# Kernel tuning notes

Hardware: AMD Instinct MI355X
Metric: run time of the kernel (lower is better)

Reference implementation:

```python
import jax, jax.numpy as jnp
import numpy as np

N_NODES = 50000


def gcn_conv(x, src, dst, W, b, n):
    # PyG GCNConv: h = x @ W; out[i] = sum_j norm_ij * h[j] + b, with added self-loops
    h = x @ W  # [N, out]
    deg = jax.ops.segment_sum(jnp.ones_like(dst, dtype=h.dtype), dst, num_segments=n)
    inv_sqrt_deg = jnp.where(deg > 0, jax.lax.rsqrt(deg), 0.0)  # [N]
    coeff = inv_sqrt_deg[src] * inv_sqrt_deg[dst]  # [E]
    msg = h[src] * coeff[:, None]  # [E, out] gather (memory-bound)
    out = jax.ops.segment_sum(msg, dst, num_segments=n)  # scatter-add
    return out + b


def setup_inputs() -> dict:
    key = jax.random.key(0)
    ks = jax.random.split(key, 8)
    n, e, c_in, c_hid, c_out = N_NODES, 800000, 128, 128, 64
    x = jax.random.normal(ks[0], (n, c_in), dtype=jnp.float32)
    edge_index = jax.random.randint(ks[1], (2, e), 0, n, dtype=jnp.int64)
    # Glorot-ish scaled weights
    W1 = jax.random.normal(ks[2], (c_in, c_hid), dtype=jnp.float32) / np.sqrt(c_in)
    b1 = jnp.zeros((c_hid,), dtype=jnp.float32)
    W2 = jax.random.normal(ks[3], (c_hid, c_out), dtype=jnp.float32) / np.sqrt(c_hid)
    b2 = jnp.zeros((c_out,), dtype=jnp.float32)
    lin_W = jax.random.normal(ks[4], (2 * c_out, c_out), dtype=jnp.float32) / np.sqrt(2 * c_out)
    lin_b = jnp.zeros((c_out,), dtype=jnp.float32)
    return {"x": x, "edge_index": edge_index, "W1": W1, "b1": b1,
            "W2": W2, "b2": b2, "lin_W": lin_W, "lin_b": lin_b}


def reference(x, edge_index, W1, b1, W2, b2, lin_W, lin_b):
    n = x.shape[0]
    # add self-loops (as GCNConv does by default)
    loops = jnp.arange(n, dtype=edge_index.dtype)
    src = jnp.concatenate([edge_index[0], loops])
    dst = jnp.concatenate([edge_index[1], loops])

    def branch(x):
        h = jax.nn.relu(gcn_conv(x, src, dst, W1, b1, n))
        # dropout: identity in eval mode (training=False)
        return gcn_conv(h, src, dst, W2, b2, n)

    x1 = branch(x)
    x2 = branch(x)
    # FusionMethod == 'Concat'
    fused = jnp.concatenate([x1, x2], axis=1) @ lin_W + lin_b
    return jax.nn.log_softmax(fused, axis=1)
```

## Files before the change

kernel.cpp:

```cpp
#include <hip/hip_runtime.h>


#define CIN  128
#define CHID 128
#define COUT 64
#define BCAP_SH 13
#define BINCHUNK 2048
#define CELLCAP 32
#define ENTCAP  5120

typedef short v8s __attribute__((ext_vector_type(8)));
typedef float v4f __attribute__((ext_vector_type(4)));

static __device__ __forceinline__ unsigned short f2bf(float f) {
    unsigned int u = __float_as_uint(f);
    unsigned int r = (u + 0x7fffu + ((u >> 16) & 1u)) >> 16;
    return (unsigned short)r;
}
static __device__ __forceinline__ float bflo(unsigned int u) {
    return __uint_as_float(u << 16);
}
static __device__ __forceinline__ float bfhi(unsigned int u) {
    return __uint_as_float(u & 0xffff0000u);
}
static __device__ __forceinline__ unsigned int pk2(float a, float b) {
    return (unsigned int)f2bf(a) | ((unsigned int)f2bf(b) << 16);
}

__global__ __launch_bounds__(256) void bin_wprep_kernel(
        const int* __restrict__ src, const int* __restrict__ dst,
        int* __restrict__ cnt, unsigned int* __restrict__ binned, int E, int nchunk,
        const float* __restrict__ W1, const float* __restrict__ W2,
        const float* __restrict__ b2, const float* __restrict__ linW,
        const float* __restrict__ linb, unsigned short* __restrict__ Wt1,
        unsigned short* __restrict__ Wt2, float* __restrict__ bp) {
    int bb = blockIdx.x;
    int t = threadIdx.x;
    if (bb < nchunk) {
        __shared__ int h[256];
        __shared__ int cur[256];
        h[t] = 0;
        __syncthreads();
        int e0 = bb * BINCHUNK;
        int e1 = e0 + BINCHUNK; if (e1 > E) e1 = E;
        for (int e = e0 + t; e < e1; e += 256)
            atomicAdd(&h[dst[e] >> 8], 1);
        __syncthreads();
        int c = h[t];
        cnt[bb * 256 + t] = c < CELLCAP ? c : CELLCAP;
        cur[t] = 0;
        __syncthreads();
        for (int e = e0 + t; e < e1; e += 256) {
            int d = dst[e];
            int b = d >> 8;
            int pos = atomicAdd(&cur[b], 1);
            if (pos < CELLCAP)
                binned[((size_t)(bb * 256 + b)) * CELLCAP + pos] =
                    (unsigned int)src[e] | (((unsigned int)d & 255u) << 16);
        }
    } else {
        int wb = bb - nchunk;
        if (wb < CHID) {
            if (t < 128) {
                Wt1[wb * CIN + t] = f2bf(W1[t * CHID + wb]);
                if (t < COUT) {
                    float acc = 0.f;
#pragma unroll 8
                    for (int k = 0; k < COUT; ++k) {
                        float wsv = linW[k * COUT + t] + linW[(k + COUT) * COUT + t];
                        acc = fmaf(W2[wb * COUT + k], wsv, acc);
                    }
                    Wt2[t * CHID + wb] = f2bf(acc);
                }
            }
        } else {
            if (t < COUT) {
                float acc = 0.f;
#pragma unroll 8
                for (int k = 0; k < COUT; ++k) {
                    float wsv = linW[k * COUT + t] + linW[(k + COUT) * COUT + t];
                    acc = fmaf(b2[k], wsv, acc);
                }
                bp[t] = acc + linb[t];
            }
        }
    }
}

__global__ __launch_bounds__(512) void csr_gemm1_kernel(
        const unsigned int* __restrict__ binned, const int* __restrict__ cnt,
        int nchunk, int nbkt,
        int2* __restrict__ rowpair, float* __restrict__ inv,
        unsigned short* __restrict__ ebuf16,
        const float* __restrict__ x, const unsigned short* __restrict__ Wt1,
        unsigned short* __restrict__ h1t, int n) {
    int t = threadIdx.x;
    if ((int)blockIdx.x < nbkt) {
        int b = blockIdx.x;
        __shared__ int cc[512];
        __shared__ int ps[512];
        __shared__ unsigned int ent[ENTCAP];
        __shared__ int h[256];
        __shared__ int s2[256];
        int v = (t < nchunk) ? cnt[t * 256 + b] : 0;
        cc[t] = v;
        ps[t] = v;
        __syncthreads();
        for (int off = 1; off < 512; off <<= 1) {
            int u = (t >= off) ? ps[t - off] : 0;
            __syncthreads();
            ps[t] += u;
            __syncthreads();
        }
        int total = ps[511];
        if (total > ENTCAP) total = ENTCAP;
        if (t < nchunk && v > 0) {
            int basei = ps[t] - v;
            const unsigned int* cell = binned + ((size_t)(t * 256 + b)) * CELLCAP;
            for (int i = 0; i < v; ++i)
                if (basei + i < ENTCAP) ent[basei + i] = cell[i];
        }
        if (t < 256) h[t] = 0;
        __syncthreads();
        for (int i = t; i < total; i += 512)
            atomicAdd(&h[ent[i] >> 16], 1);
        __syncthreads();
        int myc = (t < 256) ? h[t] : 0;
        if (t < 256) s2[t] = myc;
        __syncthreads();
        for (int off = 1; off < 256; off <<= 1) {
            int u = (t >= off && t < 256) ? s2[t - off] : 0;
            __syncthreads();
            if (t < 256) s2[t] += u;
            __syncthreads();
        }
        int base = b << BCAP_SH;
        if (t < 256) {
            int excl = s2[t] - myc;
            int node = (b << 8) + t;
            if (node < n) {
                rowpair[node] = make_int2(base + excl, base + excl + myc);
                inv[node] = rsqrtf((float)(myc + 1));
            }
            h[t] = base + excl;
        }
        __syncthreads();
        for (int i = t; i < total; i += 512) {
            unsigned int e = ent[i];
            int pos = atomicAdd(&h[e >> 16], 1);
            ebuf16[pos] = (unsigned short)(e & 0xffffu);
        }
    } else {
        int bid = blockIdx.x - nbkt;
        int lane = t & 63, wave = t >> 6;
        int quad = lane >> 4, r16 = lane & 15;
        int row0 = (bid * 8 + wave) * 16;
        if (row0 >= n) return;
        int arow = row0 + r16;
        if (arow >= n) arow = n - 1;
        size_t n32 = (size_t)n * 32;

        v4f acc[8];
#pragma unroll
        for (int c = 0; c < 8; ++c) acc[c] = (v4f){0.f, 0.f, 0.f, 0.f};
#pragma unroll
        for (int kc = 0; kc < 4; ++kc) {
            const float4* ap = (const float4*)(x + (size_t)arow * 128 + kc * 32 + quad * 8);
            float4 a0 = ap[0], a1 = ap[1];
            v8s af;
            af[0] = (short)f2bf(a0.x); af[1] = (short)f2bf(a0.y);
            af[2] = (short)f2bf(a0.z); af[3] = (short)f2bf(a0.w);
            af[4] = (short)f2bf(a1.x); af[5] = (short)f2bf(a1.y);
            af[6] = (short)f2bf(a1.z); af[7] = (short)f2bf(a1.w);
#pragma unroll
            for (int ct = 0; ct < 8; ++ct) {
                v8s bf = *(const v8s*)(Wt1 + (size_t)(ct * 16 + r16) * 128 + kc * 32 + quad * 8);
                acc[ct] = __builtin_amdgcn_mfma_f32_16x16x32_bf16(af, bf, acc[ct], 0, 0, 0);
            }
        }
#pragma unroll
        for (int ct = 0; ct < 8; ++ct) {
            int col = ct * 16 + r16;
            int pl = col >> 5, d = col & 31;
#pragma unroll
            for (int i = 0; i < 4; ++i) {
                int orow = row0 + quad * 4 + i;
                if (orow < n)
                    h1t[(size_t)pl * n32 + (size_t)orow * 32 + d] = f2bf(acc[ct][i]);
            }
        }
    }
}

__global__ __launch_bounds__(256) void agg1_slice_kernel(
        const unsigned short* __restrict__ h1t,
        const unsigned short* __restrict__ ebuf16,
        const int2* __restrict__ rowpair,
        const float* __restrict__ inv,
        const float* __restrict__ b1,
        unsigned int* __restrict__ agg1b,
        int n) {
    int b = blockIdx.x;
    int xcd = b & 7;
    int slice = xcd >> 1;
    int sub = xcd & 1;
    int grp = b >> 3;
    int wid = threadIdx.x >> 6;
    int lane = threadIdx.x & 63;
    int g = lane >> 3, s = lane & 7;
    const uint2* __restrict__ plane = (const uint2*)(h1t + (size_t)slice * n * 32);

    int node = (grp * 2 + sub) * 32 + wid * 8 + g;
    int cnode = node < n ? node : n - 1;
    int2 rp = rowpair[cnode];
    int beg = rp.x, len = rp.y - rp.x;
    int m = len < 64 ? len : 64;
    uint2 usl = plane[(size_t)cnode * 8 + s];
    float wd = inv[cnode];
    float4 bv = ((const float4*)b1)[slice * 8 + s];

    int kmax = (m + 1) & ~1;
    float a0 = 0.f, a1 = 0.f, a2 = 0.f, a3 = 0.f;
    int g8 = g << 3;
    int eid = 0;
    for (int k = 0; k < kmax; k += 2) {
        if ((k & 7) == 0) eid = (int)ebuf16[beg + k + s];
        int sa = __shfl(eid, g8 + (k & 7), 64);
        int sb = __shfl(eid, g8 + (k & 7) + 1, 64);
        sb = (k + 1 < m) ? sb : cnode;
        float iva = inv[sa], ivb = inv[sb];
        uint2 ua = plane[(size_t)sa * 8 + s];
        uint2 ub = plane[(size_t)sb * 8 + s];
        a0 = fmaf(iva, bflo(ua.x), a0); a1 = fmaf(iva, bfhi(ua.x), a1);
        a2 = fmaf(iva, bflo(ua.y), a2); a3 = fmaf(iva, bfhi(ua.y), a3);
        a0 = fmaf(ivb, bflo(ub.x), a0); a1 = fmaf(ivb, bfhi(ub.x), a1);
        a2 = fmaf(ivb, bflo(ub.y), a2); a3 = fmaf(ivb, bfhi(ub.y), a3);
    }
    if (len > 64) {
        for (int k = 64; k < len; ++k) {
            int sid = (int)ebuf16[beg + k];
            float iv2 = inv[sid];
            uint2 u = plane[(size_t)sid * 8 + s];
            a0 = fmaf(iv2, bflo(u.x), a0); a1 = fmaf(iv2, bfhi(u.x), a1);
            a2 = fmaf(iv2, bflo(u.y), a2); a3 = fmaf(iv2, bfhi(u.y), a3);
        }
    }
    float c2 = (1.0f - (float)(kmax - m)) * wd;
    a0 = fmaf(c2, bflo(usl.x), a0); a1 = fmaf(c2, bfhi(usl.x), a1);
    a2 = fmaf(c2, bflo(usl.y), a2); a3 = fmaf(c2, bfhi(usl.y), a3);
    float o0 = fmaxf(fmaf(wd, a0, bv.x), 0.f);
    float o1 = fmaxf(fmaf(wd, a1, bv.y), 0.f);
    float o2 = fmaxf(fmaf(wd, a2, bv.z), 0.f);
    float o3 = fmaxf(fmaf(wd, a3, bv.w), 0.f);
    if (node < n) {
        uint2 w; w.x = pk2(o0, o1); w.y = pk2(o2, o3);
        ((uint2*)agg1b)[(size_t)node * 32 + slice * 8 + s] = w;
    }
}

__global__ __launch_bounds__(256) void gemm2_kernel(const unsigned short* __restrict__ A,
                                                    const unsigned short* __restrict__ Wt,
                                                    const float* __restrict__ inv,
                                                    unsigned short* __restrict__ h2t, int n) {
    int lane = threadIdx.x & 63;
    int wave = threadIdx.x >> 6;
    int quad = lane >> 4, r16 = lane & 15;
    int row0 = (blockIdx.x * 4 + wave) * 16;
    if (row0 >= n) return;
    int arow = row0 + r16;
    if (arow >= n) arow = n - 1;

    v4f acc[4];
#pragma unroll
    for (int c = 0; c < 4; ++c) acc[c] = (v4f){0.f, 0.f, 0.f, 0.f};
#pragma unroll
    for (int kc = 0; kc < 4; ++kc) {
        v8s af = *(const v8s*)(A + (size_t)arow * 128 + kc * 32 + quad * 8);
#pragma unroll
        for (int ct = 0; ct < 4; ++ct) {
            v8s bf = *(const v8s*)(Wt + (size_t)(ct * 16 + r16) * 128 + kc * 32 + quad * 8);
            acc[ct] = __builtin_amdgcn_mfma_f32_16x16x32_bf16(af, bf, acc[ct], 0, 0, 0);
        }
    }
    float4 iv = ((const float4*)(inv + row0))[quad];
#pragma unroll
    for (int ct = 0; ct < 4; ++ct) {
#pragma unroll
        for (int i = 0; i < 4; ++i) {
            int orow = row0 + quad * 4 + i;
            if (orow < n) {
                float sc = (i == 0) ? iv.x : (i == 1) ? iv.y : (i == 2) ? iv.z : iv.w;
                h2t[(size_t)orow * 64 + ct * 16 + r16] = f2bf(acc[ct][i] * sc);
            }
        }
    }
}

__global__ __launch_bounds__(256) void agg2_softmax_kernel(
        const unsigned short* __restrict__ h2t,
        const unsigned short* __restrict__ ebuf16,
        const int2* __restrict__ rowpair,
        const float* __restrict__ inv,
        const float* __restrict__ bp,
        float* __restrict__ outp, int n) {
    int wid = threadIdx.x >> 6;
    int lane = threadIdx.x & 63;
    int g = lane >> 3, s = lane & 7;
    int node = blockIdx.x * 32 + wid * 8 + g;
    int cnode = node < n ? node : n - 1;
    int2 rp = rowpair[cnode];
    int beg = rp.x, len = rp.y - rp.x;
    int m = len < 64 ? len : 64;
    const uint4* __restrict__ rows = (const uint4*)h2t;
    uint4 usl = rows[(size_t)cnode * 8 + s];
    float wd = inv[cnode];

    int kmax = (m + 1) & ~1;
    float a0 = 0.f, a1 = 0.f, a2 = 0.f, a3 = 0.f;
    float a4 = 0.f, a5 = 0.f, a6 = 0.f, a7 = 0.f;
    int g8 = g << 3;
    int eid = 0;
    for (int k = 0; k < kmax; k += 2) {
        if ((k & 7) == 0) eid = (int)ebuf16[beg + k + s];
        int sa = __shfl(eid, g8 + (k & 7), 64);
        int sb = __shfl(eid, g8 + (k & 7) + 1, 64);
        sb = (k + 1 < m) ? sb : cnode;
        uint4 ua = rows[(size_t)sa * 8 + s];
        uint4 ub = rows[(size_t)sb * 8 + s];
        a0 += bflo(ua.x); a1 += bfhi(ua.x); a2 += bflo(ua.y); a3 += bfhi(ua.y);
        a4 += bflo(ua.z); a5 += bfhi(ua.z); a6 += bflo(ua.w); a7 += bfhi(ua.w);
        a0 += bflo(ub.x); a1 += bfhi(ub.x); a2 += bflo(ub.y); a3 += bfhi(ub.y);
        a4 += bflo(ub.z); a5 += bfhi(ub.z); a6 += bflo(ub.w); a7 += bfhi(ub.w);
    }
    if (len > 64) {
        for (int k = 64; k < len; ++k) {
            int sid = (int)ebuf16[beg + k];
            uint4 u = rows[(size_t)sid * 8 + s];
            a0 += bflo(u.x); a1 += bfhi(u.x); a2 += bflo(u.y); a3 += bfhi(u.y);
            a4 += bflo(u.z); a5 += bfhi(u.z); a6 += bflo(u.w); a7 += bfhi(u.w);
        }
    }
    float c2 = 1.0f - (float)(kmax - m);
    a0 = fmaf(c2, bflo(usl.x), a0); a1 = fmaf(c2, bfhi(usl.x), a1);
    a2 = fmaf(c2, bflo(usl.y), a2); a3 = fmaf(c2, bfhi(usl.y), a3);
    a4 = fmaf(c2, bflo(usl.z), a4); a5 = fmaf(c2, bfhi(usl.z), a5);
    a6 = fmaf(c2, bflo(usl.w), a6); a7 = fmaf(c2, bfhi(usl.w), a7);
    float4 bpa = ((const float4*)bp)[s * 2];
    float4 bpb = ((const float4*)bp)[s * 2 + 1];
    float f0 = fmaf(wd, a0, bpa.x), f1 = fmaf(wd, a1, bpa.y);
    float f2 = fmaf(wd, a2, bpa.z), f3 = fmaf(wd, a3, bpa.w);
    float f4 = fmaf(wd, a4, bpb.x), f5 = fmaf(wd, a5, bpb.y);
    float f6 = fmaf(wd, a6, bpb.z), f7 = fmaf(wd, a7, bpb.w);
    float mx = fmaxf(fmaxf(fmaxf(f0, f1), fmaxf(f2, f3)),
                     fmaxf(fmaxf(f4, f5), fmaxf(f6, f7)));
    mx = fmaxf(mx, __shfl_xor(mx, 1, 64));
    mx = fmaxf(mx, __shfl_xor(mx, 2, 64));
    mx = fmaxf(mx, __shfl_xor(mx, 4, 64));
    float sum = expf(f0 - mx) + expf(f1 - mx) + expf(f2 - mx) + expf(f3 - mx)
              + expf(f4 - mx) + expf(f5 - mx) + expf(f6 - mx) + expf(f7 - mx);
    sum += __shfl_xor(sum, 1, 64);
    sum += __shfl_xor(sum, 2, 64);
    sum += __shfl_xor(sum, 4, 64);
    float ls = mx + logf(sum);
    if (node < n) {
        float4 w0 = make_float4(f0 - ls, f1 - ls, f2 - ls, f3 - ls);
        float4 w1 = make_float4(f4 - ls, f5 - ls, f6 - ls, f7 - ls);
        ((float4*)outp)[(size_t)node * 16 + s * 2]     = w0;
        ((float4*)outp)[(size_t)node * 16 + s * 2 + 1] = w1;
    }
}

static inline size_t align16(size_t x) { return (x + 15) & ~(size_t)15; }

extern "C" void kernel_launch(void* const* d_in, const int* in_sizes, int n_in,
                              void* d_out, int out_size, void* d_ws, size_t ws_size,
                              hipStream_t stream) {
    const float* x    = (const float*)d_in[0];
    const int*   eidx = (const int*)d_in[1];
    const float* W1   = (const float*)d_in[2];
    const float* b1   = (const float*)d_in[3];
    const float* W2   = (const float*)d_in[4];
    const float* b2   = (const float*)d_in[5];
    const float* linW = (const float*)d_in[6];
    const float* linb = (const float*)d_in[7];
    float* out = (float*)d_out;

    const int n = in_sizes[0] / CIN;
    const int E = in_sizes[1] / 2;
    const int* src = eidx;
    const int* dst = eidx + E;
    const int NBKT = (n + 255) >> 8;
    const int NCHUNK = (E + BINCHUNK - 1) / BINCHUNK;

    char* ws = (char*)d_ws;
    size_t off = 0;
    int2*  rowpair = (int2*)(ws + off);  off = align16(off + (size_t)n * 8);
    float* inv     = (float*)(ws + off); off = align16(off + (size_t)n * 4);
    int*   cnt     = (int*)(ws + off);   off = align16(off + (size_t)NCHUNK * 256 * 4);
    unsigned short* Wt1 = (unsigned short*)(ws + off); off = align16(off + (size_t)CHID * CIN * 2);
    unsigned short* Wt2 = (unsigned short*)(ws + off); off = align16(off + (size_t)COUT * CHID * 2);
    float* bp      = (float*)(ws + off); off = align16(off + (size_t)COUT * 4);
    unsigned int* binned = (unsigned int*)(ws + off);
    off = align16(off + (size_t)NCHUNK * 256 * CELLCAP * 4);
    unsigned short* ebuf16 = (unsigned short*)(ws + off);
    off = align16(off + (size_t)256 * (1 << BCAP_SH) * 2);
    unsigned short* h1t   = (unsigned short*)(ws + off); off = align16(off + (size_t)n * CHID * 2);
    unsigned int*   agg1b = (unsigned int*)(ws + off);   off = align16(off + (size_t)n * CHID * 2);
    unsigned short* h2t   = (unsigned short*)(ws + off); off = align16(off + (size_t)n * COUT * 2);

    bin_wprep_kernel<<<NCHUNK + CHID + 1, 256, 0, stream>>>(
        src, dst, cnt, binned, E, NCHUNK, W1, W2, b2, linW, linb, Wt1, Wt2, bp);

    const int G1B = (n + 127) / 128;
    csr_gemm1_kernel<<<NBKT + G1B, 512, 0, stream>>>(
        binned, cnt, NCHUNK, NBKT, rowpair, inv, ebuf16, x, Wt1, h1t, n);

    const int NG1 = (n + 63) / 64;
    agg1_slice_kernel<<<NG1 * 8, 256, 0, stream>>>(h1t, ebuf16, rowpair, inv, b1, agg1b, n);

    gemm2_kernel<<<(n + 63) / 64, 256, 0, stream>>>((const unsigned short*)agg1b, Wt2, inv, h2t, n);

    agg2_softmax_kernel<<<(n + 31) / 32, 256, 0, stream>>>(h2t, ebuf16, rowpair, inv, bp, out, n);
}
```

Measured before the change: 191.6 us.

## Split CSR and GEMM1 kernels, prescale h1 rows by inverse sqrt degree

Separates the fused CSR-build and first GEMM into two launches so GEMM1 can run after the inverse-sqrt-degree array is ready. GEMM1 then multiplies each output row by its source normalisation, which lets the first aggregation drop the per-neighbour inv[] gather and just sum rows. The aggregation loop is widened to four neighbours per iteration to expose more memory parallelism. The cost is an extra kernel launch and serialisation that removes the overlap the fused kernel had between CSR construction and GEMM1.

```diff
diff --git a/kernel.cpp b/kernel.cpp
--- a/kernel.cpp
+++ b/kernel.cpp
@@ -73,120 +73,120 @@
                     Wt2[t * CHID + wb] = f2bf(acc);
                 }
             }
-        } else {
-            if (t < COUT) {
-                float acc = 0.f;
+        } else if (t < COUT) {
+            float acc = 0.f;
 #pragma unroll 8
-                for (int k = 0; k < COUT; ++k) {
-                    float wsv = linW[k * COUT + t] + linW[(k + COUT) * COUT + t];
-                    acc = fmaf(b2[k], wsv, acc);
-                }
-                bp[t] = acc + linb[t];
+            for (int k = 0; k < COUT; ++k) {
+                float wsv = linW[k * COUT + t] + linW[(k + COUT) * COUT + t];
+                acc = fmaf(b2[k], wsv, acc);
             }
-        }
-    }
-}
-
-__global__ __launch_bounds__(512) void csr_gemm1_kernel(
+            bp[t] = acc + linb[t];
+        }
+    }
+}
+
+__global__ __launch_bounds__(512) void csr_kernel(
         const unsigned int* __restrict__ binned, const int* __restrict__ cnt,
-        int nchunk, int nbkt,
+        int nchunk,
         int2* __restrict__ rowpair, float* __restrict__ inv,
-        unsigned short* __restrict__ ebuf16,
-        const float* __restrict__ x, const unsigned short* __restrict__ Wt1,
-        unsigned short* __restrict__ h1t, int n) {
+        unsigned short* __restrict__ ebuf16, int n) {
+    int b = blockIdx.x;
     int t = threadIdx.x;
-    if ((int)blockIdx.x < nbkt) {
-        int b = blockIdx.x;
-        __shared__ int cc[512];
-        __shared__ int ps[512];
-        __shared__ unsigned int ent[ENTCAP];
-        __shared__ int h[256];
-        __shared__ int s2[256];
-        int v = (t < nchunk) ? cnt[t * 256 + b] : 0;
-        cc[t] = v;
-        ps[t] = v;
-        __syncthreads();
-        for (int off = 1; off < 512; off <<= 1) {
-            int u = (t >= off) ? ps[t - off] : 0;
-            __syncthreads();
-            ps[t] += u;
-            __syncthreads();
-        }
-        int total = ps[511];
-        if (total > ENTCAP) total = ENTCAP;
-        if (t < nchunk && v > 0) {
-            int basei = ps[t] - v;
-            const unsigned int* cell = binned + ((size_t)(t * 256 + b)) * CELLCAP;
-            for (int i = 0; i < v; ++i)
-                if (basei + i < ENTCAP) ent[basei + i] = cell[i];
-        }
-        if (t < 256) h[t] = 0;
-        __syncthreads();
-        for (int i = t; i < total; i += 512)
-            atomicAdd(&h[ent[i] >> 16], 1);
-        __syncthreads();
-        int myc = (t < 256) ? h[t] : 0;
-        if (t < 256) s2[t] = myc;
-        __syncthreads();
-        for (int off = 1; off < 256; off <<= 1) {
-            int u = (t >= off && t < 256) ? s2[t - off] : 0;
-            __syncthreads();
-            if (t < 256) s2[t] += u;
-            __syncthreads();
-        }
-        int base = b << BCAP_SH;
-        if (t < 256) {
-            int excl = s2[t] - myc;
-            int node = (b << 8) + t;
-            if (node < n) {
-                rowpair[node] = make_int2(base + excl, base + excl + myc);
-                inv[node] = rsqrtf((float)(myc + 1));
-            }
-            h[t] = base + excl;
-        }
-        __syncthreads();
-        for (int i = t; i < total; i += 512) {
-            unsigned int e = ent[i];
-            int pos = atomicAdd(&h[e >> 16], 1);
-            ebuf16[pos] = (unsigned short)(e & 0xffffu);
-        }
-    } else {
-        int bid = blockIdx.x - nbkt;
-        int lane = t & 63, wave = t >> 6;
-        int quad = lane >> 4, r16 = lane & 15;
-        int row0 = (bid * 8 + wave) * 16;
-        if (row0 >= n) return;
-        int arow = row0 + r16;
-        if (arow >= n) arow = n - 1;
-        size_t n32 = (size_t)n * 32;
-
-        v4f acc[8];
-#pragma unroll
-        for (int c = 0; c < 8; ++c) acc[c] = (v4f){0.f, 0.f, 0.f, 0.f};
-#pragma unroll
-        for (int kc = 0; kc < 4; ++kc) {
-            const float4* ap = (const float4*)(x + (size_t)arow * 128 + kc * 32 + quad * 8);
-            float4 a0 = ap[0], a1 = ap[1];
-            v8s af;
-            af[0] = (short)f2bf(a0.x); af[1] = (short)f2bf(a0.y);
-            af[2] = (short)f2bf(a0.z); af[3] = (short)f2bf(a0.w);
-            af[4] = (short)f2bf(a1.x); af[5] = (short)f2bf(a1.y);
-            af[6] = (short)f2bf(a1.z); af[7] = (short)f2bf(a1.w);
-#pragma unroll
-            for (int ct = 0; ct < 8; ++ct) {
-                v8s bf = *(const v8s*)(Wt1 + (size_t)(ct * 16 + r16) * 128 + kc * 32 + quad * 8);
-                acc[ct] = __builtin_amdgcn_mfma_f32_16x16x32_bf16(af, bf, acc[ct], 0, 0, 0);
-            }
-        }
+    __shared__ int ps[512];
+    __shared__ unsigned int ent[ENTCAP];
+    __shared__ int h[256];
+    __shared__ int s2[256];
+    int v = (t < nchunk) ? cnt[t * 256 + b] : 0;
+    ps[t] = v;
+    __syncthreads();
+    for (int off = 1; off < 512; off <<= 1) {
+        int u = (t >= off) ? ps[t - off] : 0;
+        __syncthreads();
+        ps[t] += u;
+        __syncthreads();
+    }
+    int total = ps[511];
+    if (total > ENTCAP) total = ENTCAP;
+    if (t < nchunk && v > 0) {
+        int basei = ps[t] - v;
+        const unsigned int* cell = binned + ((size_t)(t * 256 + b)) * CELLCAP;
+        for (int i = 0; i < v; ++i)
+            if (basei + i < ENTCAP) ent[basei + i] = cell[i];
+    }
+    if (t < 256) h[t] = 0;
+    __syncthreads();
+    for (int i = t; i < total; i += 512)
+        atomicAdd(&h[ent[i] >> 16], 1);
+    __syncthreads();
+    int myc = (t < 256) ? h[t] : 0;
+    if (t < 256) s2[t] = myc;
+    __syncthreads();
+    for (int off = 1; off < 256; off <<= 1) {
+        int u = (t >= off && t < 256) ? s2[t - off] : 0;
+        __syncthreads();
+        if (t < 256) s2[t] += u;
+        __syncthreads();
+    }
+    int base = b << BCAP_SH;
+    if (t < 256) {
+        int excl = s2[t] - myc;
+        int node = (b << 8) + t;
+        if (node < n) {
+            rowpair[node] = make_int2(base + excl, base + excl + myc);
+            inv[node] = rsqrtf((float)(myc + 1));
+        }
+        h[t] = base + excl;
+    }
+    __syncthreads();
+    for (int i = t; i < total; i += 512) {
+        unsigned int e = ent[i];
+        int pos = atomicAdd(&h[e >> 16], 1);
+        ebuf16[pos] = (unsigned short)(e & 0xffffu);
+    }
+}
+
+__global__ __launch_bounds__(256) void gemm1_kernel(const float* __restrict__ A,
+                                                    const unsigned short* __restrict__ Wt,
+                                                    const float* __restrict__ inv,
+                                                    unsigned short* __restrict__ h1t, int n) {
+    int lane = threadIdx.x & 63;
+    int wave = threadIdx.x >> 6;
+    int quad = lane >> 4, r16 = lane & 15;
+    int row0 = (blockIdx.x * 4 + wave) * 16;
+    if (row0 >= n) return;
+    int arow = row0 + r16;
+    if (arow >= n) arow = n - 1;
+    size_t n32 = (size_t)n * 32;
+
+    v4f acc[8];
+#pragma unroll
+    for (int c = 0; c < 8; ++c) acc[c] = (v4f){0.f, 0.f, 0.f, 0.f};
+#pragma unroll
+    for (int kc = 0; kc < 4; ++kc) {
+        const float4* ap = (const float4*)(A + (size_t)arow * 128 + kc * 32 + quad * 8);
+        float4 a0 = ap[0], a1 = ap[1];
+        v8s af;
+        af[0] = (short)f2bf(a0.x); af[1] = (short)f2bf(a0.y);
+        af[2] = (short)f2bf(a0.z); af[3] = (short)f2bf(a0.w);
+        af[4] = (short)f2bf(a1.x); af[5] = (short)f2bf(a1.y);
+        af[6] = (short)f2bf(a1.z); af[7] = (short)f2bf(a1.w);
 #pragma unroll
         for (int ct = 0; ct < 8; ++ct) {
-            int col = ct * 16 + r16;
-            int pl = col >> 5, d = col & 31;
-#pragma unroll
-            for (int i = 0; i < 4; ++i) {
-                int orow = row0 + quad * 4 + i;
-                if (orow < n)
-                    h1t[(size_t)pl * n32 + (size_t)orow * 32 + d] = f2bf(acc[ct][i]);
+            v8s bf = *(const v8s*)(Wt + (size_t)(ct * 16 + r16) * 128 + kc * 32 + quad * 8);
+            acc[ct] = __builtin_amdgcn_mfma_f32_16x16x32_bf16(af, bf, acc[ct], 0, 0, 0);
+        }
+    }
+    float4 iv = ((const float4*)(inv + row0))[quad];
+#pragma unroll
+    for (int ct = 0; ct < 8; ++ct) {
+        int col = ct * 16 + r16;
+        int pl = col >> 5, d = col & 31;
+#pragma unroll
+        for (int i = 0; i < 4; ++i) {
+            int orow = row0 + quad * 4 + i;
+            if (orow < n) {
+                float sc = (i == 0) ? iv.x : (i == 1) ? iv.y : (i == 2) ? iv.z : iv.w;
+                h1t[(size_t)pl * n32 + (size_t)orow * 32 + d] = f2bf(acc[ct][i] * sc);
             }
         }
     }
@@ -208,6 +208,7 @@
     int wid = threadIdx.x >> 6;
     int lane = threadIdx.x & 63;
     int g = lane >> 3, s = lane & 7;
+    int g8 = g << 3;
     const uint2* __restrict__ plane = (const uint2*)(h1t + (size_t)slice * n * 32);
 
     int node = (grp * 2 + sub) * 32 + wid * 8 + g;
@@ -219,35 +220,38 @@
     float wd = inv[cnode];
     float4 bv = ((const float4*)b1)[slice * 8 + s];
 
-    int kmax = (m + 1) & ~1;
+    int kmax = (m + 3) & ~3;
     float a0 = 0.f, a1 = 0.f, a2 = 0.f, a3 = 0.f;
-    int g8 = g << 3;
     int eid = 0;
-    for (int k = 0; k < kmax; k += 2) {
+    for (int k = 0; k < kmax; k += 4) {
         if ((k & 7) == 0) eid = (int)ebuf16[beg + k + s];
-        int sa = __shfl(eid, g8 + (k & 7), 64);
-        int sb = __shfl(eid, g8 + (k & 7) + 1, 64);
-        sb = (k + 1 < m) ? sb : cnode;
-        float iva = inv[sa], ivb = inv[sb];
-        uint2 ua = plane[(size_t)sa * 8 + s];
-        uint2 ub = plane[(size_t)sb * 8 + s];
-        a0 = fmaf(iva, bflo(ua.x), a0); a1 = fmaf(iva, bfhi(ua.x), a1);
-        a2 = fmaf(iva, bflo(ua.y), a2); a3 = fmaf(iva, bfhi(ua.y), a3);
-        a0 = fmaf(ivb, bflo(ub.x), a0); a1 = fmaf(ivb, bfhi(ub.x), a1);
-        a2 = fmaf(ivb, bflo(ub.y), a2); a3 = fmaf(ivb, bfhi(ub.y), a3);
+        int i0 = __shfl(eid, g8 + (k & 7) + 0, 64);
+        int i1 = __shfl(eid, g8 + (k & 7) + 1, 64);
+        int i2 = __shfl(eid, g8 + (k & 7) + 2, 64);
+        int i3 = __shfl(eid, g8 + (k & 7) + 3, 64);
+        i0 = (k     < m) ? i0 : cnode;
+        i1 = (k + 1 < m) ? i1 : cnode;
+        i2 = (k + 2 < m) ? i2 : cnode;
+        i3 = (k + 3 < m) ? i3 : cnode;
+        uint2 u0 = plane[(size_t)i0 * 8 + s];
+        uint2 u1 = plane[(size_t)i1 * 8 + s];
+        uint2 u2 = plane[(size_t)i2 * 8 + s];
+        uint2 u3 = plane[(size_t)i3 * 8 + s];
+        a0 += bflo(u0.x); a1 += bfhi(u0.x); a2 += bflo(u0.y); a3 += bfhi(u0.y);
+        a0 += bflo(u1.x); a1 += bfhi(u1.x); a2 += bflo(u1.y); a3 += bfhi(u1.y);
+        a0 += bflo(u2.x); a1 += bfhi(u2.x); a2 += bflo(u2.y); a3 += bfhi(u2.y);
+        a0 += bflo(u3.x); a1 += bfhi(u3.x); a2 += bflo(u3.y); a3 += bfhi(u3.y);
     }
     if (len > 64) {
         for (int k = 64; k < len; ++k) {
             int sid = (int)ebuf16[beg + k];
-            float iv2 = inv[sid];
-            uint2 u = plane[(size_t)sid * 8 + s];
-            a0 = fmaf(iv2, bflo(u.x), a0); a1 = fmaf(iv2, bfhi(u.x), a1);
-            a2 = fmaf(iv2, bflo(u.y), a2); a3 = fmaf(iv2, bfhi(u.y), a3);
-        }
-    }
-    float c2 = (1.0f - (float)(kmax - m)) * wd;
-    a0 = fmaf(c2, bflo(usl.x), a0); a1 = fmaf(c2, bfhi(usl.x), a1);
-    a2 = fmaf(c2, bflo(usl.y), a2); a3 = fmaf(c2, bfhi(usl.y), a3);
+            uint2 uu = plane[(size_t)sid * 8 + s];
+            a0 += bflo(uu.x); a1 += bfhi(uu.x); a2 += bflo(uu.y); a3 += bfhi(uu.y);
+        }
+    }
+    float cc = 1.0f - (float)(kmax - m);
+    a0 = fmaf(cc, bflo(usl.x), a0); a1 = fmaf(cc, bfhi(usl.x), a1);
+    a2 = fmaf(cc, bflo(usl.y), a2); a3 = fmaf(cc, bfhi(usl.y), a3);
     float o0 = fmaxf(fmaf(wd, a0, bv.x), 0.f);
     float o1 = fmaxf(fmaf(wd, a1, bv.y), 0.f);
     float o2 = fmaxf(fmaf(wd, a2, bv.z), 0.f);
@@ -306,6 +310,7 @@
     int wid = threadIdx.x >> 6;
     int lane = threadIdx.x & 63;
     int g = lane >> 3, s = lane & 7;
+    int g8 = g << 3;
     int node = blockIdx.x * 32 + wid * 8 + g;
     int cnode = node < n ? node : n - 1;
     int2 rp = rowpair[cnode];
@@ -318,12 +323,12 @@
     int kmax = (m + 1) & ~1;
     float a0 = 0.f, a1 = 0.f, a2 = 0.f, a3 = 0.f;
     float a4 = 0.f, a5 = 0.f, a6 = 0.f, a7 = 0.f;
-    int g8 = g << 3;
     int eid = 0;
     for (int k = 0; k < kmax; k += 2) {
         if ((k & 7) == 0) eid = (int)ebuf16[beg + k + s];
         int sa = __shfl(eid, g8 + (k & 7), 64);
         int sb = __shfl(eid, g8 + (k & 7) + 1, 64);
+        sa = (k     < m) ? sa : cnode;
         sb = (k + 1 < m) ? sb : cnode;
         uint4 ua = rows[(size_t)sa * 8 + s];
         uint4 ub = rows[(size_t)sb * 8 + s];
@@ -363,10 +368,10 @@
     sum += __shfl_xor(sum, 4, 64);
     float ls = mx + logf(sum);
     if (node < n) {
-        float4 w0 = make_float4(f0 - ls, f1 - ls, f2 - ls, f3 - ls);
-        float4 w1 = make_float4(f4 - ls, f5 - ls, f6 - ls, f7 - ls);
-        ((float4*)outp)[(size_t)node * 16 + s * 2]     = w0;
-        ((float4*)outp)[(size_t)node * 16 + s * 2 + 1] = w1;
+        ((float4*)outp)[(size_t)node * 16 + s * 2] =
+            make_float4(f0 - ls, f1 - ls, f2 - ls, f3 - ls);
+        ((float4*)outp)[(size_t)node * 16 + s * 2 + 1] =
+            make_float4(f4 - ls, f5 - ls, f6 - ls, f7 - ls);
     }
 }
 
@@ -411,9 +416,9 @@
     bin_wprep_kernel<<<NCHUNK + CHID + 1, 256, 0, stream>>>(
         src, dst, cnt, binned, E, NCHUNK, W1, W2, b2, linW, linb, Wt1, Wt2, bp);
 
-    const int G1B = (n + 127) / 128;
-    csr_gemm1_kernel<<<NBKT + G1B, 512, 0, stream>>>(
-        binned, cnt, NCHUNK, NBKT, rowpair, inv, ebuf16, x, Wt1, h1t, n);
+    csr_kernel<<<NBKT, 512, 0, stream>>>(binned, cnt, NCHUNK, rowpair, inv, ebuf16, n);
+
+    gemm1_kernel<<<(n + 63) / 64, 256, 0, stream>>>(x, Wt1, inv, h1t, n);
 
     const int NG1 = (n + 63) / 64;
     agg1_slice_kernel<<<NG1 * 8, 256, 0, stream>>>(h1t, ebuf16, rowpair, inv, b1, agg1b, n);
```

Result: no change. 192.0 us (+0.2%).
